# Performance work log

Hardware: AMD Instinct MI355X
Metric: run time of the kernel (lower is better)

The kernel has to match this reference:

```python
import jax, jax.numpy as jnp
import numpy as np

B, S, MD, H = 8, 1024, 1024, 16
D = MD // H  # 64
# Faithful to torch: scale = (dim_per_head // num_heads) ** -0.5 (a quirk, not 1/sqrt(D))
SCALE = float((D // H) ** (-0.5))


def setup_inputs() -> dict:
    k0 = jax.random.key(0)
    ks = jax.random.split(k0, 11)
    w = 1.0 / np.sqrt(MD)
    mk = lambda k, shape, s: jax.random.normal(k, shape, dtype=jnp.float32) * s
    return {
        "query": mk(ks[0], (B, S, MD), 1.0),
        "key": mk(ks[1], (B, S, MD), 1.0),
        "value": mk(ks[2], (B, S, MD), 1.0),
        "Wq": mk(ks[3], (MD, MD), w), "bq": mk(ks[4], (MD,), w),
        "Wk": mk(ks[5], (MD, MD), w), "bk": mk(ks[6], (MD,), w),
        "Wv": mk(ks[7], (MD, MD), w), "bv": mk(ks[8], (MD,), w),
        "Wo": mk(ks[9], (MD, MD), w), "bo": mk(ks[10], (MD,), w),
    }


def reference(query, key, value, Wq, bq, Wk, bk, Wv, bv, Wo, bo):
    # Dropout is identity in eval mode (deterministic reference).
    Bq, T, _ = query.shape
    Sk = key.shape[1]
    q = query @ Wq + bq   # [B, T, H*D]
    k = key @ Wk + bk     # [B, S, H*D]
    v = value @ Wv + bv
    # Faithful replication of torch .view(B*H, -1, D): plain row-major reshape
    # (NOT a head transpose -- it chunks sequence/head indices together).
    q = q.reshape(Bq * H, T, D)
    k = k.reshape(Bq * H, Sk, D)
    v = v.reshape(Bq * H, Sk, D)
    attn = jnp.einsum('btd,bsd->bts', q, k) * SCALE          # [B*H, T, S]
    p = jax.nn.softmax(attn, axis=-1)
    ctx = jnp.einsum('bts,bsd->btd', p, v).reshape(Bq, T, H * D)
    output = ctx @ Wo + bo                                    # [B, T, MD]
    a = attn.reshape(Bq, H, T, Sk)
    attn_post = jax.nn.sigmoid(a).sum(axis=1) / H             # [B, T, S]
    return output, attn_post
```

## Files before the change

### kernel.cpp

```cpp
#include <hip/hip_runtime.h>


typedef __attribute__((ext_vector_type(8))) short bf16x8;
typedef __attribute__((ext_vector_type(4))) float f32x4;

static __device__ __forceinline__ short f2bf(float f) {
  union { float f; unsigned u; } v; v.f = f;
  unsigned lsb = (v.u >> 16) & 1u;
  v.u += 0x7fffu + lsb;
  return (short)(v.u >> 16);
}

static __device__ __forceinline__ short f2bf_rhu(float f) {
  union { float f; unsigned u; } v; v.f = f;
  v.u += 0x8000u;
  return (short)(v.u >> 16);
}

static __device__ __forceinline__ float exp2_hw(float x) {
  float r;
  asm("v_exp_f32 %0, %1" : "=v"(r) : "v"(x));
  return r;
}

#define L2E_HALF 0.72134752f

#define GLDS16(gp, lp) __builtin_amdgcn_global_load_lds( \
    (const __attribute__((address_space(1))) void*)(gp), \
    (__attribute__((address_space(3))) void*)(lp), 16, 0, 0)

struct Ptr4 { const float* s[4]; short* d[4]; };
struct Ptr3 { const float* s[3]; short* d[3]; };
struct QkvArgs { const short* A[3]; const short* B[3]; const float* bias[3]; short* C[3]; };

__global__ __launch_bounds__(256) void convt4(Ptr4 a)
{
  const float* __restrict__ src = a.s[blockIdx.z];
  short* __restrict__ dst = a.d[blockIdx.z];
  __shared__ float T[64][65];
  const int tid = threadIdx.x;
  const int c0 = blockIdx.x * 64, r0 = blockIdx.y * 64;
  {
    const int rr = tid >> 4, cc = (tid & 15) * 4;
    for (int i = 0; i < 4; ++i) {
      int row = rr + i * 16;
      const float4 v = *(const float4*)(src + (size_t)(r0 + row) * 1024 + c0 + cc);
      T[row][cc] = v.x; T[row][cc + 1] = v.y; T[row][cc + 2] = v.z; T[row][cc + 3] = v.w;
    }
  }
  __syncthreads();
  {
    const int rr = tid >> 3, cc = (tid & 7) * 8;
    for (int i = 0; i < 2; ++i) {
      int row = rr + i * 32;
      bf16x8 v;
      for (int j = 0; j < 8; ++j) v[j] = f2bf(T[cc + j][row]);
      *(bf16x8*)(dst + (size_t)(c0 + row) * 1024 + r0 + cc) = v;
    }
  }
}

__global__ __launch_bounds__(256) void cvt3(Ptr3 a)
{
  const float* __restrict__ src = a.s[blockIdx.z];
  short* __restrict__ dst = a.d[blockIdx.z];
  const size_t i = ((size_t)blockIdx.x * 256 + threadIdx.x) * 8;
  const float4 v0 = *(const float4*)(src + i);
  const float4 v1 = *(const float4*)(src + i + 4);
  bf16x8 o;
  o[0] = f2bf(v0.x); o[1] = f2bf(v0.y); o[2] = f2bf(v0.z); o[3] = f2bf(v0.w);
  o[4] = f2bf(v1.x); o[5] = f2bf(v1.y); o[6] = f2bf(v1.z); o[7] = f2bf(v1.w);
  *(bf16x8*)(dst + i) = o;
}

__global__ __launch_bounds__(256) void transp_v(
    const short* __restrict__ src, short* __restrict__ dst)
{
  __shared__ short T[64][72];
  const int g = blockIdx.y, t0 = blockIdx.x * 64;
  const short* s = src + (size_t)g * 65536 + (size_t)t0 * 64;
  short* d = dst + (size_t)g * 65536 + t0;
  const int r = threadIdx.x >> 3, c = (threadIdx.x & 7) * 8;
  for (int i = 0; i < 2; ++i) {
    bf16x8 v = *(const bf16x8*)(s + (size_t)(r + i * 32) * 64 + c);
    *(bf16x8*)(&T[r + i * 32][c]) = v;
  }
  __syncthreads();
  for (int i = 0; i < 2; ++i) {
    int dr = r + i * 32;
    bf16x8 v;
    for (int j = 0; j < 8; ++j) v[j] = T[c + j][dr];
    *(bf16x8*)(d + (size_t)dr * 1024 + c) = v;
  }
}

static __device__ __forceinline__ void gemm_body(
    const short* __restrict__ A, const short* __restrict__ BT,
    const float* __restrict__ bias, void* __restrict__ Cp, int mode)
{
  __shared__ short As[128 * 64];
  __shared__ short Bs[128 * 64];
  const int K = 1024, N = 1024;
  const int tid = threadIdx.x;
  const int lane = tid & 63, wave = tid >> 6;
  const int quad = lane >> 4, l16 = lane & 15;
  const int wm = (wave & 1) * 64, wn = (wave >> 1) * 64;
  const int lin = blockIdx.y * 64 + blockIdx.x;
  const int bx = (lin >> 3) & 63;
  const int by = lin & 7;
  const int bm = bx * 128, bn = by * 128;

  f32x4 acc[4][4] = {};

  const int s_row = tid >> 3;
  const int s_col = (tid & 7) * 8;
  const int lds_base = wave * 512;

  for (int k0 = 0; k0 < K; k0 += 64) {
    for (int i = 0; i < 4; ++i) {
      int row = s_row + i * 32;
      GLDS16(A + (size_t)(bm + row) * K + k0 + s_col, &As[i * 2048 + lds_base]);
      GLDS16(BT + (size_t)(bn + row) * K + k0 + s_col, &Bs[i * 2048 + lds_base]);
    }
    __syncthreads();
    for (int ks = 0; ks < 2; ++ks) {
      bf16x8 af[4], bfr[4];
      for (int mi = 0; mi < 4; ++mi)
        af[mi] = *(const bf16x8*)(&As[(wm + mi * 16 + l16) * 64 + ks * 32 + quad * 8]);
      for (int ni = 0; ni < 4; ++ni)
        bfr[ni] = *(const bf16x8*)(&Bs[(wn + ni * 16 + l16) * 64 + ks * 32 + quad * 8]);
      for (int mi = 0; mi < 4; ++mi)
        for (int ni = 0; ni < 4; ++ni)
          acc[mi][ni] = __builtin_amdgcn_mfma_f32_16x16x32_bf16(af[mi], bfr[ni], acc[mi][ni], 0, 0, 0);
    }
    __syncthreads();
  }

  for (int ni = 0; ni < 4; ++ni) {
    int col = bn + wn + ni * 16 + l16;
    float bv = bias[col];
    for (int mi = 0; mi < 4; ++mi) {
      int row0 = bm + wm + mi * 16 + quad * 4;
      for (int r = 0; r < 4; ++r) {
        int row = row0 + r;
        float fv = acc[mi][ni][r] + bv;
        if (mode == 2) ((float*)Cp)[(size_t)row * N + col] = fv;
        else           ((short*)Cp)[(size_t)row * N + col] = f2bf(fv);
      }
    }
  }
}

__global__ __launch_bounds__(256) void gemm_bt16(
    const short* __restrict__ A, const short* __restrict__ BT,
    const float* __restrict__ bias, void* __restrict__ Cp, int mode)
{
  gemm_body(A, BT, bias, Cp, mode);
}

__global__ __launch_bounds__(256) void gemm_qkv(QkvArgs a)
{
  const int z = blockIdx.z;
  gemm_body(a.A[z], a.B[z], a.bias[z], a.C[z], 0);
}

__global__ __launch_bounds__(256, 1) void attn_fused8(
    const short* __restrict__ Qp, const short* __restrict__ Kp,
    const short* __restrict__ VpT,
    short* __restrict__ ctx,
    float* __restrict__ attn_post)
{
  __shared__ short Plds[32][1032];
  __shared__ float red[32][4];

  const int tid = threadIdx.x;
  const int wave = tid >> 6, lane = tid & 63;
  const int quad = lane >> 4, l16 = lane & 15;
  const int orig = blockIdx.x;
  const int b = orig & 7;
  const int t0 = (orig >> 3) * 32;
  const int sbase = wave * 256;

  float sig[2][16][4] = {};

  for (int h = 0; h < 16; ++h) {
    const int g = b * 16 + h;
    const short* Qg = Qp + (size_t)g * 65536;
    const short* Kg = Kp + (size_t)g * 65536;
    const short* Vg = VpT + (size_t)g * 65536;

    bf16x8 aq[2][2];
#pragma unroll
    for (int tt = 0; tt < 2; ++tt) {
      aq[tt][0] = *(const bf16x8*)(Qg + (t0 + tt * 16 + l16) * 64 + quad * 8);
      aq[tt][1] = *(const bf16x8*)(Qg + (t0 + tt * 16 + l16) * 64 + 32 + quad * 8);
    }

    float rsum[2][4] = {};

    bf16x8 kb0[4], kb1[4];
#pragma unroll
    for (int t = 0; t < 4; ++t) {
      int s = sbase + t * 16;
      kb0[t] = *(const bf16x8*)(Kg + (s + l16) * 64 + quad * 8);
      kb1[t] = *(const bf16x8*)(Kg + (s + l16) * 64 + 32 + quad * 8);
    }
#pragma unroll
    for (int tile = 0; tile < 16; ++tile) {
      const int slot = tile & 3;
      bf16x8 bk0 = kb0[slot], bk1 = kb1[slot];
      if (tile < 12) {
        int s = sbase + (tile + 4) * 16;
        kb0[slot] = *(const bf16x8*)(Kg + (s + l16) * 64 + quad * 8);
        kb1[slot] = *(const bf16x8*)(Kg + (s + l16) * 64 + 32 + quad * 8);
      }
#pragma unroll
      for (int tt = 0; tt < 2; ++tt) {
        f32x4 c = {0.f, 0.f, 0.f, 0.f};
        c = __builtin_amdgcn_mfma_f32_16x16x32_bf16(aq[tt][0], bk0, c, 0, 0, 0);
        c = __builtin_amdgcn_mfma_f32_16x16x32_bf16(aq[tt][1], bk1, c, 0, 0, 0);
#pragma unroll
        for (int r = 0; r < 4; ++r) {
          float e = exp2_hw(c[r] * L2E_HALF);
          rsum[tt][r] += e;
          Plds[tt * 16 + quad * 4 + r][sbase + tile * 16 + l16] = f2bf_rhu(e);
          sig[tt][tile][r] += e * __builtin_amdgcn_rcpf(1.f + e);
        }
      }
    }
#pragma unroll
    for (int tt = 0; tt < 2; ++tt)
      for (int r = 0; r < 4; ++r)
        for (int mask = 1; mask < 16; mask <<= 1)
          rsum[tt][r] += __shfl_xor(rsum[tt][r], mask, 64);
    if (l16 == 0)
#pragma unroll
      for (int tt = 0; tt < 2; ++tt)
        for (int r = 0; r < 4; ++r)
          red[tt * 16 + quad * 4 + r][wave] = rsum[tt][r];
    __syncthreads();

    const short* Vw = Vg + (size_t)(wave * 16 + l16) * 1024;
    f32x4 acc[2][2] = {};
#pragma unroll
    for (int sl = 0; sl < 32; ++sl) {
      bf16x8 v  = *(const bf16x8*)(Vw + sl * 32 + quad * 8);
      bf16x8 p0 = *(const bf16x8*)(&Plds[l16][sl * 32 + quad * 8]);
      bf16x8 p1 = *(const bf16x8*)(&Plds[16 + l16][sl * 32 + quad * 8]);
      acc[0][sl & 1] = __builtin_amdgcn_mfma_f32_16x16x32_bf16(p0, v, acc[0][sl & 1], 0, 0, 0);
      acc[1][sl & 1] = __builtin_amdgcn_mfma_f32_16x16x32_bf16(p1, v, acc[1][sl & 1], 0, 0, 0);
    }

    short* ctxg = ctx + (size_t)g * 65536 + t0 * 64;
#pragma unroll
    for (int tt = 0; tt < 2; ++tt)
      for (int r = 0; r < 4; ++r) {
        int row = tt * 16 + quad * 4 + r;
        float s4 = red[row][0] + red[row][1] + red[row][2] + red[row][3];
        float inv = __builtin_amdgcn_rcpf(s4);
        float cval = (acc[tt][0][r] + acc[tt][1][r]) * inv;
        ctxg[row * 64 + wave * 16 + l16] = f2bf(cval);
      }
    __syncthreads();
  }

  float* ap_out = attn_post + (size_t)b * 1048576 + (size_t)t0 * 1024;
#pragma unroll
  for (int tt = 0; tt < 2; ++tt)
    for (int tile = 0; tile < 16; ++tile)
      for (int r = 0; r < 4; ++r)
        ap_out[(tt * 16 + quad * 4 + r) * 1024 + sbase + tile * 16 + l16] =
            sig[tt][tile][r] * 0.0625f;
}

extern "C" void kernel_launch(void* const* d_in, const int* in_sizes, int n_in,
                              void* d_out, int out_size, void* d_ws, size_t ws_size,
                              hipStream_t stream) {
  const float* query = (const float*)d_in[0];
  const float* key   = (const float*)d_in[1];
  const float* value = (const float*)d_in[2];
  const float* Wq = (const float*)d_in[3]; const float* bq = (const float*)d_in[4];
  const float* Wk = (const float*)d_in[5]; const float* bk = (const float*)d_in[6];
  const float* Wv = (const float*)d_in[7]; const float* bv = (const float*)d_in[8];
  const float* Wo = (const float*)d_in[9]; const float* bo = (const float*)d_in[10];

  float* out0 = (float*)d_out;
  float* attn_post = out0 + (8u << 20);

  short* WqT = (short*)d_ws;
  short* WkT = WqT + (1u << 20);
  short* WvT = WkT + (1u << 20);
  short* WoT = WvT + (1u << 20);
  short* Qp  = WoT + (1u << 20);
  short* Kp  = Qp + (8u << 20);
  short* VpT = Kp + (8u << 20);

  dim3 blk(256);
  const size_t NEED_BIG = (size_t)(60u << 20) * 2;

  convt4<<<dim3(16, 16, 4), blk, 0, stream>>>(
      Ptr4{{Wq, Wk, Wv, Wo}, {WqT, WkT, WvT, WoT}});

  short* ctx;
  if (ws_size >= NEED_BIG) {
    short* Xq = VpT + (8u << 20);
    short* Xk = Xq + (8u << 20);
    short* Xv = Xk + (8u << 20);
    short* Vflat = Xv + (8u << 20);
    ctx = Xq;

    cvt3<<<dim3(4096, 1, 3), blk, 0, stream>>>(Ptr3{{query, key, value}, {Xq, Xk, Xv}});
    gemm_qkv<<<dim3(64, 8, 3), blk, 0, stream>>>(
        QkvArgs{{Xq, Xk, Xv}, {WqT, WkT, WvT}, {bq, bk, bv}, {Qp, Kp, Vflat}});
    transp_v<<<dim3(16, 128), blk, 0, stream>>>(Vflat, VpT);
  } else {
    short* Xin = VpT + (8u << 20);
    short* Vflat = Xin + (8u << 20);
    ctx = Xin;

    cvt3<<<dim3(4096, 1, 1), blk, 0, stream>>>(Ptr3{{query, query, query}, {Xin, Xin, Xin}});
    gemm_bt16<<<dim3(64, 8), blk, 0, stream>>>(Xin, WqT, bq, Qp, 0);
    cvt3<<<dim3(4096, 1, 1), blk, 0, stream>>>(Ptr3{{key, key, key}, {Xin, Xin, Xin}});
    gemm_bt16<<<dim3(64, 8), blk, 0, stream>>>(Xin, WkT, bk, Kp, 0);
    cvt3<<<dim3(4096, 1, 1), blk, 0, stream>>>(Ptr3{{value, value, value}, {Xin, Xin, Xin}});
    gemm_bt16<<<dim3(64, 8), blk, 0, stream>>>(Xin, WvT, bv, Vflat, 0);
    transp_v<<<dim3(16, 128), blk, 0, stream>>>(Vflat, VpT);
  }

  attn_fused8<<<dim3(256), blk, 0, stream>>>(Qp, Kp, VpT, ctx, attn_post);
  gemm_bt16<<<dim3(64, 8), blk, 0, stream>>>(ctx, WoT, bo, out0, 2);
}
```

Before: 445.7 us.

## Double-buffer LDS tiles in GEMM body and remap blocks for XCD locality

The shared GEMM body now uses two LDS buffers, so the next K-tile's global-to-LDS loads are issued while MFMAs run on the current tile, leaving one barrier per iteration instead of two. The block-to-tile mapping is also changed so that blocks landing on the same XCD cover a contiguous group of 8 M-tiles, which is meant to improve L2 reuse of A and B rows. In exchange, LDS use per block doubles to 64 KB, which may lower occupancy.

```diff
diff --git a/kernel.cpp b/kernel.cpp
--- a/kernel.cpp
+++ b/kernel.cpp
@@ -98,16 +98,17 @@
     const short* __restrict__ A, const short* __restrict__ BT,
     const float* __restrict__ bias, void* __restrict__ Cp, int mode)
 {
-  __shared__ short As[128 * 64];
-  __shared__ short Bs[128 * 64];
+  __shared__ short As[2][128 * 64];
+  __shared__ short Bs[2][128 * 64];
   const int K = 1024, N = 1024;
   const int tid = threadIdx.x;
   const int lane = tid & 63, wave = tid >> 6;
   const int quad = lane >> 4, l16 = lane & 15;
   const int wm = (wave & 1) * 64, wn = (wave >> 1) * 64;
   const int lin = blockIdx.y * 64 + blockIdx.x;
-  const int bx = (lin >> 3) & 63;
-  const int by = lin & 7;
+  const int xcd = lin & 7, idx = lin >> 3;
+  const int bx = xcd * 8 + (idx & 7);
+  const int by = idx >> 3;
   const int bm = bx * 128, bn = by * 128;
 
   f32x4 acc[4][4] = {};
@@ -116,24 +117,35 @@
   const int s_col = (tid & 7) * 8;
   const int lds_base = wave * 512;
 
-  for (int k0 = 0; k0 < K; k0 += 64) {
-    for (int i = 0; i < 4; ++i) {
-      int row = s_row + i * 32;
-      GLDS16(A + (size_t)(bm + row) * K + k0 + s_col, &As[i * 2048 + lds_base]);
-      GLDS16(BT + (size_t)(bn + row) * K + k0 + s_col, &Bs[i * 2048 + lds_base]);
-    }
-    __syncthreads();
+  for (int i = 0; i < 4; ++i) {
+    int row = s_row + i * 32;
+    GLDS16(A + (size_t)(bm + row) * K + s_col, &As[0][i * 2048 + lds_base]);
+    GLDS16(BT + (size_t)(bn + row) * K + s_col, &Bs[0][i * 2048 + lds_base]);
+  }
+  __syncthreads();
+
+  int cur = 0;
+  for (int t = 0; t < 16; ++t) {
+    if (t < 15) {
+      const int k0 = (t + 1) * 64;
+      for (int i = 0; i < 4; ++i) {
+        int row = s_row + i * 32;
+        GLDS16(A + (size_t)(bm + row) * K + k0 + s_col, &As[cur ^ 1][i * 2048 + lds_base]);
+        GLDS16(BT + (size_t)(bn + row) * K + k0 + s_col, &Bs[cur ^ 1][i * 2048 + lds_base]);
+      }
+    }
     for (int ks = 0; ks < 2; ++ks) {
       bf16x8 af[4], bfr[4];
       for (int mi = 0; mi < 4; ++mi)
-        af[mi] = *(const bf16x8*)(&As[(wm + mi * 16 + l16) * 64 + ks * 32 + quad * 8]);
+        af[mi] = *(const bf16x8*)(&As[cur][(wm + mi * 16 + l16) * 64 + ks * 32 + quad * 8]);
       for (int ni = 0; ni < 4; ++ni)
-        bfr[ni] = *(const bf16x8*)(&Bs[(wn + ni * 16 + l16) * 64 + ks * 32 + quad * 8]);
+        bfr[ni] = *(const bf16x8*)(&Bs[cur][(wn + ni * 16 + l16) * 64 + ks * 32 + quad * 8]);
       for (int mi = 0; mi < 4; ++mi)
         for (int ni = 0; ni < 4; ++ni)
           acc[mi][ni] = __builtin_amdgcn_mfma_f32_16x16x32_bf16(af[mi], bfr[ni], acc[mi][ni], 0, 0, 0);
     }
     __syncthreads();
+    cur ^= 1;
   }
 
   for (int ni = 0; ni < 4; ++ni) {
@@ -296,6 +308,7 @@
   short* VpT = Kp + (8u << 20);
 
   dim3 blk(256);
+  dim3 ggrid(64, 8);
   const size_t NEED_BIG = (size_t)(60u << 20) * 2;
 
   convt4<<<dim3(16, 16, 4), blk, 0, stream>>>(
@@ -319,14 +332,14 @@
     ctx = Xin;
 
     cvt3<<<dim3(4096, 1, 1), blk, 0, stream>>>(Ptr3{{query, query, query}, {Xin, Xin, Xin}});
-    gemm_bt16<<<dim3(64, 8), blk, 0, stream>>>(Xin, WqT, bq, Qp, 0);
+    gemm_bt16<<<ggrid, blk, 0, stream>>>(Xin, WqT, bq, Qp, 0);
     cvt3<<<dim3(4096, 1, 1), blk, 0, stream>>>(Ptr3{{key, key, key}, {Xin, Xin, Xin}});
-    gemm_bt16<<<dim3(64, 8), blk, 0, stream>>>(Xin, WkT, bk, Kp, 0);
+    gemm_bt16<<<ggrid, blk, 0, stream>>>(Xin, WkT, bk, Kp, 0);
     cvt3<<<dim3(4096, 1, 1), blk, 0, stream>>>(Ptr3{{value, value, value}, {Xin, Xin, Xin}});
-    gemm_bt16<<<dim3(64, 8), blk, 0, stream>>>(Xin, WvT, bv, Vflat, 0);
+    gemm_bt16<<<ggrid, blk, 0, stream>>>(Xin, WvT, bv, Vflat, 0);
     transp_v<<<dim3(16, 128), blk, 0, stream>>>(Vflat, VpT);
   }
 
   attn_fused8<<<dim3(256), blk, 0, stream>>>(Qp, Kp, VpT, ctx, attn_post);
-  gemm_bt16<<<dim3(64, 8), blk, 0, stream>>>(ctx, WoT, bo, out0, 2);
-}
+  gemm_bt16<<<ggrid, blk, 0, stream>>>(ctx, WoT, bo, out0, 2);
+}
```

After: 455.6 us, median of 2. 2.2% more time.
